# Kernel tuning notes

Measured on AMD Instinct MI355X. Metric: run time of the kernel, lower is better.

Reference implementation:

```python
import jax, jax.numpy as jnp
import numpy as np

Q, B, DM, H, HD, MEM = 1024, 4, 1024, 16, 64, 512
KLEN = MEM + Q
MLP = 4096
SCALE = 1.0 / np.sqrt(HD)
EPS = 1e-5


def _layer_norm(x, g, b):
    m = jnp.mean(x, axis=-1, keepdims=True)
    var = jnp.mean(jnp.square(x - m), axis=-1, keepdims=True)
    return (x - m) * jax.lax.rsqrt(var + EPS) * g + b


def _rel_shift(x):
    # x: [qlen, klen, batch, heads] -> Transformer-XL relative shift
    q, k, b, h = x.shape
    x = jnp.pad(x, ((0, 0), (1, 0), (0, 0), (0, 0)))  # [q, k+1, b, h]
    x = x.reshape(k + 1, q, b, h)[1:]                  # drop first row
    return x.reshape(q, k, b, h)


def setup_inputs() -> dict:
    key = jax.random.key(0)
    ks = jax.random.split(key, 16)
    s = 0.02
    inputs = jax.random.normal(ks[0], (Q, B, DM), jnp.float32)
    r = jax.random.normal(ks[1], (KLEN, DM), jnp.float32)
    u = jax.random.normal(ks[2], (H, HD), jnp.float32) * s
    v = jax.random.normal(ks[3], (H, HD), jnp.float32) * s
    mem = jax.random.normal(ks[4], (MEM, B, DM), jnp.float32)
    # causal mask with memory: query i may attend to keys j <= i + MEM
    i = jnp.arange(Q)[:, None]
    j = jnp.arange(KLEN)[None, :]
    attn_mask = j > (i + MEM)  # True = masked
    W_qkv = jax.random.normal(ks[5], (DM, 3 * H * HD), jnp.float32) * s
    W_r = jax.random.normal(ks[6], (DM, H * HD), jnp.float32) * s
    W_o = jax.random.normal(ks[7], (H * HD, DM), jnp.float32) * s
    ln1_g = jnp.ones((DM,), jnp.float32)
    ln1_b = jnp.zeros((DM,), jnp.float32)
    ln2_g = jnp.ones((DM,), jnp.float32)
    ln2_b = jnp.zeros((DM,), jnp.float32)
    W1 = jax.random.normal(ks[8], (DM, MLP), jnp.float32) * s
    b1 = jnp.zeros((MLP,), jnp.float32)
    W2 = jax.random.normal(ks[9], (MLP, DM), jnp.float32) * s
    b2 = jnp.zeros((DM,), jnp.float32)
    return {"inputs": inputs, "r": r, "u": u, "v": v, "mem": mem,
            "attn_mask": attn_mask, "W_qkv": W_qkv, "W_r": W_r, "W_o": W_o,
            "ln1_g": ln1_g, "ln1_b": ln1_b, "ln2_g": ln2_g, "ln2_b": ln2_b,
            "W1": W1, "b1": b1, "W2": W2, "b2": b2}


def reference(inputs, r, u, v, mem, attn_mask, W_qkv, W_r, W_o,
              ln1_g, ln1_b, ln2_g, ln2_b, W1, b1, W2, b2):
    qlen = inputs.shape[0]
    cat = jnp.concatenate([mem, inputs], axis=0)      # [klen, B, DM]
    klen = cat.shape[0]
    qkv = cat @ W_qkv                                  # [klen, B, 3*H*HD]
    q_h, k_h, v_h = jnp.split(qkv, 3, axis=-1)
    q_h = q_h[-qlen:].reshape(qlen, -1, H, HD)         # [q, B, H, HD]
    k_h = k_h.reshape(klen, -1, H, HD)                 # [k, B, H, HD]
    v_h = v_h.reshape(klen, -1, H, HD)
    r_h = (r @ W_r).reshape(klen, H, HD)               # [k, H, HD]
    # content score (AC) + position score (BD, rel-shifted)
    AC = jnp.einsum('ibhd,jbhd->ijbh', q_h + u, k_h)
    BD = _rel_shift(jnp.einsum('ibhd,jhd->ijbh', q_h + v, r_h))
    score = (AC + BD) * SCALE                          # [q, k, B, H]
    score = jnp.where(attn_mask[:, :, None, None], jnp.float32(-1e30), score)
    attn = jax.nn.softmax(score, axis=1)
    ctx = jnp.einsum('ijbh,jbhd->ibhd', attn, v_h).reshape(qlen, -1, H * HD)
    y = ctx @ W_o                                      # [q, B, DM]
    x = _layer_norm(inputs + y, ln1_g, ln1_b)
    h = jax.nn.relu(x @ W1 + b1)
    y2 = h @ W2 + b2
    return _layer_norm(x + y2, ln2_g, ln2_b)
```

## Files before the change

### kernel.cpp

```cpp
#include <hip/hip_runtime.h>
#include <hip/hip_bf16.h>

typedef __hip_bfloat16 bf16;
typedef _Float16 f16;
typedef __attribute__((ext_vector_type(8))) short short8;
typedef __attribute__((ext_vector_type(4))) float f32x4;
typedef __attribute__((ext_vector_type(8))) _Float16 f16x8;
typedef __attribute__((ext_vector_type(4))) _Float16 f16x4;

#define Q_LEN 1024
#define B_SZ 4
#define DM 1024
#define H_CNT 16
#define HD 64
#define MEM_LEN 512
#define KLEN 1536
#define MLP 4096

__device__ __forceinline__ void store_c(float* p, float v) { *p = v; }
__device__ __forceinline__ void store_c(bf16* p, float v) { *p = __float2bfloat16(v); }
__device__ __forceinline__ void store_c(f16* p, float v) { *p = (f16)v; }

__device__ __forceinline__ float b2f(short s) {
  union { unsigned u; float f; } x;
  x.u = ((unsigned)(unsigned short)s) << 16;
  return x.f;
}
__device__ __forceinline__ short f2b(float f) {
  union { float f; unsigned u; } x;
  x.f = f;
  unsigned r = x.u + 0x7fff + ((x.u >> 16) & 1);
  return (short)(r >> 16);
}

__device__ __forceinline__ void gload16(const void* g, void* l) {
  __builtin_amdgcn_global_load_lds(
      (__attribute__((address_space(1))) unsigned int*)(g),
      (__attribute__((address_space(3))) unsigned int*)(l), 16, 0, 0);
}

__global__ __launch_bounds__(256) void convh_kernel(
    const float* __restrict__ X, f16* __restrict__ Y, int n4) {
  const int i = blockIdx.x * 256 + threadIdx.x;
  if (i < n4) {
    f32x4 v = *(const f32x4*)&X[(size_t)i * 4];
    f16x4 h;
#pragma unroll
    for (int j = 0; j < 4; ++j) h[j] = (f16)v[j];
    *(f16x4*)&Y[(size_t)i * 4] = h;
  }
}

__global__ __launch_bounds__(256) void convT_kernel(
    const float* __restrict__ W, f16* __restrict__ WT, int K, int N) {
  __shared__ float tile[64][65];
  const int tid = threadIdx.x;
  const int k0 = blockIdx.y * 64, n0 = blockIdx.x * 64;
  const int tn = tid & 63, tk4 = tid >> 6;
#pragma unroll
  for (int p = 0; p < 16; ++p) {
    const int kk = tk4 + p * 4;
    tile[kk][tn] = W[(size_t)(k0 + kk) * N + n0 + tn];
  }
  __syncthreads();
#pragma unroll
  for (int p = 0; p < 16; ++p) {
    const int nn = tk4 + p * 4;
    WT[(size_t)(n0 + nn) * K + k0 + tn] = (f16)tile[tn][nn];
  }
}

template <typename TC>
__global__ __launch_bounds__(256, 3) void hgemm_kernel(
    const f16* __restrict__ A, const f16* __restrict__ BT, TC* C,
    int N, int K, const float* __restrict__ bias, int relu,
    const f16* __restrict__ Aalt, TC* Calt, int split,
    TC* Cb, TC* Cbalt, int ksplit) {
  __shared__ __align__(16) f16 sA[3][128 * 32];
  __shared__ __align__(16) f16 sB[3][128 * 32];
  const int tid = threadIdx.x;
  const int w = tid >> 6, lane = tid & 63;
  const int quad = lane >> 4, m16 = lane & 15;
  const int wr = w >> 1, wc = w & 1;
  const int gx = gridDim.x;
  const int nwg = gx * gridDim.y;
  const int lin = blockIdx.y * gx + blockIdx.x;
  const int cpx = nwg >> 3;
  const int swz = (lin & 7) * cpx + (lin >> 3);
  const int bx = swz % gx;
  int by = swz / gx;
  int koff = 0, Kloc = K;
  if (ksplit == 2) {
    const int mh = gridDim.y >> 1;
    if (by >= mh) { by -= mh; koff = K >> 1; C = Cb; Calt = Cbalt; }
    Kloc = K >> 1;
  }
  const int col0 = bx * 128;
  int r0 = by * 128;
  const f16* Ause = A;
  TC* Cuse = C;
  if (r0 >= split) { Ause = Aalt; Cuse = Calt; r0 -= split; }

  const int strow = tid >> 2;
  const int schunk = tid & 3;
  const int sw = schunk ^ ((strow >> 1) & 3);
  const f16* gA0 = Ause + (size_t)(r0 + strow) * K + koff + sw * 8;
  const f16* gB0 = BT + (size_t)(col0 + strow) * K + koff + sw * 8;
  f16* ldsA0 = &sA[0][0] + (size_t)w * 512;
  f16* ldsB0 = &sB[0][0] + (size_t)w * 512;

  const int qs = quad ^ ((m16 >> 1) & 3);
  int aoff[4], boff[4];
#pragma unroll
  for (int i = 0; i < 4; ++i) {
    aoff[i] = (wr * 64 + i * 16 + m16) * 32 + qs * 8;
    boff[i] = (wc * 64 + i * 16 + m16) * 32 + qs * 8;
  }

  const int nkt = Kloc >> 5;
  f32x4 acc[4][4] = {};

  auto stage = [&](int buf, int t) {
    const int k0 = t << 5;
    const size_t bufo = (size_t)buf * 4096;
    gload16(gA0 + k0, ldsA0 + bufo);
    gload16(gA0 + (size_t)64 * K + k0, ldsA0 + bufo + 2048);
    gload16(gB0 + k0, ldsB0 + bufo);
    gload16(gB0 + (size_t)64 * K + k0, ldsB0 + bufo + 2048);
  };

  stage(0, 0);
  stage(1, 1);
  int cur = 0;
  for (int t = 0; t < nkt; ++t) {
    if (t + 1 < nkt) {
      asm volatile("s_waitcnt vmcnt(4)" ::: "memory");
    } else {
      asm volatile("s_waitcnt vmcnt(0)" ::: "memory");
    }
    __builtin_amdgcn_s_barrier();
    if (t + 2 < nkt) {
      int nb = cur + 2;
      if (nb >= 3) nb -= 3;
      stage(nb, t + 2);
    }
    f16x8 af[4], bfr[4];
#pragma unroll
    for (int i = 0; i < 4; ++i) af[i] = *(const f16x8*)&sA[cur][aoff[i]];
#pragma unroll
    for (int i = 0; i < 4; ++i) bfr[i] = *(const f16x8*)&sB[cur][boff[i]];
    __builtin_amdgcn_s_setprio(1);
#pragma unroll
    for (int mi = 0; mi < 4; ++mi)
#pragma unroll
      for (int ni = 0; ni < 4; ++ni)
        acc[mi][ni] = __builtin_amdgcn_mfma_f32_16x16x32_f16(
            af[mi], bfr[ni], acc[mi][ni], 0, 0, 0);
    __builtin_amdgcn_s_setprio(0);
    cur = (cur + 1 == 3) ? 0 : cur + 1;
  }

#pragma unroll
  for (int mi = 0; mi < 4; ++mi) {
    const int row = r0 + wr * 64 + mi * 16 + quad * 4;
#pragma unroll
    for (int ni = 0; ni < 4; ++ni) {
      const int col = col0 + wc * 64 + ni * 16 + m16;
      const float bv = bias ? bias[col] : 0.f;
#pragma unroll
      for (int rg = 0; rg < 4; ++rg) {
        float vv = acc[mi][ni][rg] + bv;
        if (relu) vv = vv > 0.f ? vv : 0.f;
        store_c(&Cuse[(size_t)(row + rg) * N + col], vv);
      }
    }
  }
}

__global__ __launch_bounds__(256, 4) void fattn_kernel(
    const bf16* __restrict__ qkvp,
    const bf16* __restrict__ rhp,
    const float* __restrict__ u, const float* __restrict__ v,
    f16* __restrict__ ctxh) {
  const int lin = blockIdx.x;
  const int p = lin & 63;
  const int b = p & 3, h = p >> 2;
  const int i0 = (15 - (lin >> 6)) * 64;
  const int tid = threadIdx.x;
  const int w = tid >> 6, lane = tid & 63;
  const int quad = lane >> 4, m16 = lane & 15;

  __shared__ short sVt[64 * 40];
  __shared__ short sR[96 * 72];
  __shared__ short sProb[64 * 40];

  const short* qkv = (const short*)qkvp;
  const short* rh  = (const short*)rhp;

  short8 aQu0, aQu1, aQv0, aQv1;
  {
    const size_t qro = ((size_t)(512 + i0 + w * 16 + m16) * 4 + b) * 3072 + h * 64 + quad * 8;
    short8 qa = *(const short8*)&qkv[qro];
    short8 qb = *(const short8*)&qkv[qro + 32];
    const float* up = u + h * 64 + quad * 8;
    const float* vp = v + h * 64 + quad * 8;
#pragma unroll
    for (int j = 0; j < 8; ++j) {
      const float qaf = b2f(qa[j]), qbf = b2f(qb[j]);
      aQu0[j] = f2b(qaf + up[j]);
      aQu1[j] = f2b(qbf + up[j + 32]);
      aQv0[j] = f2b(qaf + vp[j]);
      aQv1[j] = f2b(qbf + vp[j + 32]);
    }
  }

  const int st_row = tid >> 3, st_d0 = (tid & 7) * 8;
  const int vj = lane & 31, vd0 = w * 16 + (lane >> 5) * 8;

#pragma unroll
  for (int p_ = 0; p_ < 3; ++p_) {
    int t = 960 - i0 + p_ * 32 + st_row;
    t = t > 1535 ? 1535 : t;
    *(short8*)&sR[(p_ * 32 + st_row) * 72 + st_d0] =
        *(const short8*)&rh[(size_t)t * 1024 + h * 64 + st_d0];
  }
  {
    short8 v8 = *(const short8*)&qkv[((size_t)vj * 4 + b) * 3072 + 2048 + h * 64 + vd0];
#pragma unroll
    for (int q = 0; q < 8; ++q) sVt[(vd0 + q) * 40 + vj] = v8[q];
  }
  short8 rKf[4];
#pragma unroll
  for (int n0i = 0; n0i < 2; ++n0i) {
    const size_t kro = ((size_t)(n0i * 16 + m16) * 4 + b) * 3072 + 1024 + h * 64 + quad * 8;
    rKf[n0i * 2] = *(const short8*)&qkv[kro];
    rKf[n0i * 2 + 1] = *(const short8*)&qkv[kro + 32];
  }

  short8 ones;
#pragma unroll
  for (int q = 0; q < 8; ++q) ones[q] = (short)0x3F80;

  f32x4 O[4] = {};
  f32x4 L = {};
  float m = -1e30f;
  int bk = 0;
  int tnext = 1056 - i0;

  const int n_kt = ((i0 + 575) >> 5) + 1;
  for (int kt = 0; kt < n_kt; ++kt) {
    const int j0 = kt * 32;
    const bool pf = (kt + 1 < n_kt);
    __syncthreads();

    short8 nV, nR;
    if (pf) {
      nV = *(const short8*)&qkv[((size_t)(j0 + 32 + vj) * 4 + b) * 3072 + 2048 + h * 64 + vd0];
      int t = tnext + st_row;
      t = t > 1535 ? 1535 : t;
      nR = *(const short8*)&rh[(size_t)t * 1024 + h * 64 + st_d0];
    }

    f32x4 ac[2];
#pragma unroll
    for (int n0i = 0; n0i < 2; ++n0i) {
      f32x4 a = {};
      a = __builtin_amdgcn_mfma_f32_16x16x32_bf16(aQu0, rKf[n0i * 2], a, 0, 0, 0);
      a = __builtin_amdgcn_mfma_f32_16x16x32_bf16(aQu1, rKf[n0i * 2 + 1], a, 0, 0, 0);
      ac[n0i] = a;
    }
    if (pf) {
#pragma unroll
      for (int n0i = 0; n0i < 2; ++n0i) {
        const size_t kro = ((size_t)(j0 + 32 + n0i * 16 + m16) * 4 + b) * 3072 + 1024 + h * 64 + quad * 8;
        rKf[n0i * 2] = *(const short8*)&qkv[kro];
        rKf[n0i * 2 + 1] = *(const short8*)&qkv[kro + 32];
      }
    }

    f32x4 pb[3];
#pragma unroll
    for (int pt = 0; pt < 3; ++pt) {
      const int p0 = 48 - 16 * w + 16 * pt;
      int pr = bk + p0;
      if (pr >= 96) pr -= 96;
      int row = pr + m16;
      if (row >= 96) row -= 96;
      const short8 bR0 = *(const short8*)&sR[row * 72 + quad * 8];
      const short8 bR1 = *(const short8*)&sR[row * 72 + 32 + quad * 8];
      f32x4 pf_ = {};
      pf_ = __builtin_amdgcn_mfma_f32_16x16x32_bf16(aQv0, bR0, pf_, 0, 0, 0);
      pf_ = __builtin_amdgcn_mfma_f32_16x16x32_bf16(aQv1, bR1, pf_, 0, 0, 0);
      pb[pt] = pf_;
    }

    float S0[4], S1[4];
    float mxl = -1e30f;
#pragma unroll
    for (int rg = 0; rg < 4; ++rg) {
      const int rloc = quad * 4 + rg;
      const int irow = i0 + w * 16 + rloc;
      const int c0 = m16 - rloc + 15;
      const int src = (lane & 48) | (c0 & 15);
      const float t0 = __shfl(pb[0][rg], src);
      const float t1 = __shfl(pb[1][rg], src);
      const float t2 = __shfl(pb[2][rg], src);
      const float p0v = (c0 < 16) ? t0 : t1;
      const float p1v = (c0 < 16) ? t1 : t2;
      float s0 = (ac[0][rg] + p0v) * 0.125f;
      float s1 = (ac[1][rg] + p1v) * 0.125f;
      if (j0 + m16 > irow + 512) s0 = -1e30f;
      if (j0 + 16 + m16 > irow + 512) s1 = -1e30f;
      S0[rg] = s0;
      S1[rg] = s1;
      mxl = fmaxf(mxl, fmaxf(s0, s1));
    }
    mxl = fmaxf(mxl, __shfl_xor(mxl, 1));
    mxl = fmaxf(mxl, __shfl_xor(mxl, 2));
    mxl = fmaxf(mxl, __shfl_xor(mxl, 4));
    mxl = fmaxf(mxl, __shfl_xor(mxl, 8));
    mxl = fmaxf(mxl, __shfl_xor(mxl, 16));
    mxl = fmaxf(mxl, __shfl_xor(mxl, 32));
    const float mnew = fmaxf(m, mxl);
    const float al = __expf(m - mnew);
    m = mnew;
#pragma unroll
    for (int rg = 0; rg < 4; ++rg) {
      const int rloc = quad * 4 + rg;
      sProb[(w * 16 + rloc) * 40 + m16] = f2b(__expf(S0[rg] - mnew));
      sProb[(w * 16 + rloc) * 40 + 16 + m16] = f2b(__expf(S1[rg] - mnew));
    }
#pragma unroll
    for (int d0i = 0; d0i < 4; ++d0i)
#pragma unroll
      for (int rg = 0; rg < 4; ++rg) O[d0i][rg] *= al;
#pragma unroll
    for (int rg = 0; rg < 4; ++rg) L[rg] *= al;

    const short8 aP = *(const short8*)&sProb[(w * 16 + m16) * 40 + quad * 8];
    L = __builtin_amdgcn_mfma_f32_16x16x32_bf16(aP, ones, L, 0, 0, 0);
#pragma unroll
    for (int d0i = 0; d0i < 4; ++d0i) {
      const short8 bV = *(const short8*)&sVt[(d0i * 16 + m16) * 40 + quad * 8];
      O[d0i] = __builtin_amdgcn_mfma_f32_16x16x32_bf16(aP, bV, O[d0i], 0, 0, 0);
    }

    __syncthreads();
    if (pf) {
#pragma unroll
      for (int q = 0; q < 8; ++q) sVt[(vd0 + q) * 40 + vj] = nV[q];
      *(short8*)&sR[(bk + st_row) * 72 + st_d0] = nR;
    }
    bk += 32;
    if (bk >= 96) bk = 0;
    tnext += 32;
  }

#pragma unroll
  for (int d0i = 0; d0i < 4; ++d0i) {
#pragma unroll
    for (int rg = 0; rg < 4; ++rg) {
      const int irow = i0 + w * 16 + quad * 4 + rg;
      ctxh[((size_t)irow * 4 + b) * 1024 + h * 64 + d0i * 16 + m16] =
          (f16)(O[d0i][rg] / L[rg]);
    }
  }
}

__global__ __launch_bounds__(256) void ln1_kernel(
    const f16* __restrict__ ya, const f16* __restrict__ yb,
    const float* __restrict__ inp, const float* __restrict__ g,
    const float* __restrict__ beta, f16* __restrict__ xh) {
  const int r = blockIdx.x, tid = threadIdx.x;
  __shared__ float red[256];
  float t[4];
  float s = 0.f;
#pragma unroll
  for (int q = 0; q < 4; ++q) {
    int c = tid + q * 256;
    t[q] = (float)ya[(size_t)r * DM + c] + (float)yb[(size_t)r * DM + c] +
           inp[(size_t)r * DM + c];
    s += t[q];
  }
  red[tid] = s;
  __syncthreads();
  for (int st = 128; st > 0; st >>= 1) {
    if (tid < st) red[tid] += red[tid + st];
    __syncthreads();
  }
  const float mean = red[0] * (1.f / DM);
  __syncthreads();
  float vs = 0.f;
#pragma unroll
  for (int q = 0; q < 4; ++q) {
    float d0 = t[q] - mean;
    vs += d0 * d0;
  }
  red[tid] = vs;
  __syncthreads();
  for (int st = 128; st > 0; st >>= 1) {
    if (tid < st) red[tid] += red[tid + st];
    __syncthreads();
  }
  const float rstd = rsqrtf(red[0] * (1.f / DM) + 1e-5f);
#pragma unroll
  for (int q = 0; q < 4; ++q) {
    int c = tid + q * 256;
    const float val = (t[q] - mean) * rstd * g[c] + beta[c];
    xh[(size_t)r * DM + c] = (f16)val;
  }
}

__global__ __launch_bounds__(256) void ln2_kernel(
    const f16* __restrict__ xh, const f16* __restrict__ y2a,
    const f16* __restrict__ y2b, const float* __restrict__ b2,
    const float* __restrict__ g, const float* __restrict__ beta,
    float* __restrict__ out) {
  const int r = blockIdx.x, tid = threadIdx.x;
  __shared__ float red[256];
  float t[4];
  float s = 0.f;
#pragma unroll
  for (int q = 0; q < 4; ++q) {
    int c = tid + q * 256;
    t[q] = (float)xh[(size_t)r * DM + c] + (float)y2a[(size_t)r * DM + c] +
           (float)y2b[(size_t)r * DM + c] + b2[c];
    s += t[q];
  }
  red[tid] = s;
  __syncthreads();
  for (int st = 128; st > 0; st >>= 1) {
    if (tid < st) red[tid] += red[tid + st];
    __syncthreads();
  }
  const float mean = red[0] * (1.f / DM);
  __syncthreads();
  float vs = 0.f;
#pragma unroll
  for (int q = 0; q < 4; ++q) {
    float d0 = t[q] - mean;
    vs += d0 * d0;
  }
  red[tid] = vs;
  __syncthreads();
  for (int st = 128; st > 0; st >>= 1) {
    if (tid < st) red[tid] += red[tid + st];
    __syncthreads();
  }
  const float rstd = rsqrtf(red[0] * (1.f / DM) + 1e-5f);
#pragma unroll
  for (int q = 0; q < 4; ++q) {
    int c = tid + q * 256;
    out[(size_t)r * DM + c] = (t[q] - mean) * rstd * g[c] + beta[c];
  }
}

extern "C" void kernel_launch(void* const* d_in, const int* in_sizes, int n_in,
                              void* d_out, int out_size, void* d_ws, size_t ws_size,
                              hipStream_t stream) {
  const int o = (n_in >= 17) ? 1 : 0;
  const float* inputs = (const float*)d_in[0];
  const float* r      = (const float*)d_in[1];
  const float* u      = (const float*)d_in[2];
  const float* v      = (const float*)d_in[3];
  const float* memp   = (const float*)d_in[4];
  const float* W_qkv  = (const float*)d_in[5 + o];
  const float* W_r    = (const float*)d_in[6 + o];
  const float* W_o    = (const float*)d_in[7 + o];
  const float* ln1_g  = (const float*)d_in[8 + o];
  const float* ln1_b  = (const float*)d_in[9 + o];
  const float* ln2_g  = (const float*)d_in[10 + o];
  const float* ln2_b  = (const float*)d_in[11 + o];
  const float* W1     = (const float*)d_in[12 + o];
  const float* b1     = (const float*)d_in[13 + o];
  const float* W2     = (const float*)d_in[14 + o];
  const float* b2     = (const float*)d_in[15 + o];

  char* ws = (char*)d_ws;
  f16*  WqkvT = (f16*)(ws);
  f16*  r16   = (f16*)(ws + 6291456);
  f16*  WrT   = (f16*)(ws + 9437184);
  bf16* qkv   = (bf16*)(ws + 11534336);
  bf16* rh    = (bf16*)(ws + 49283072);
  f16*  cat_h = (f16*)d_out;
  f16*  ctx_h = (f16*)(ws);
  f16*  WoT   = (f16*)(ws + 8388608);
  f16*  ya    = (f16*)(ws + 10485760);
  f16*  yb    = (f16*)(ws + 18874368);
  f16*  x_h   = (f16*)(ws + 27262976);
  f16*  W1T   = (f16*)(ws + 35651584);
  f16*  h_hi  = (f16*)(ws);
  f16*  h_lo  = (f16*)d_out;
  f16*  W2T   = (f16*)(ws + 44040192);
  f16*  y2a   = (f16*)(ws + 18874368);
  f16*  y2b   = (f16*)(ws + 35651584);

  dim3 blk(256);
  const int BIG = 1 << 30;

  convh_kernel<<<dim3(2048), blk, 0, stream>>>(memp, cat_h, 524288);
  convh_kernel<<<dim3(4096), blk, 0, stream>>>(inputs, cat_h + (size_t)2048 * 1024, 1048576);
  convh_kernel<<<dim3(1536), blk, 0, stream>>>(r, r16, 393216);
  convT_kernel<<<dim3(48, 16), blk, 0, stream>>>(W_qkv, WqkvT, 1024, 3072);
  convT_kernel<<<dim3(16, 16), blk, 0, stream>>>(W_r, WrT, 1024, 1024);
  hgemm_kernel<bf16><<<dim3(24, 48), blk, 0, stream>>>(
      cat_h, WqkvT, qkv, 3072, 1024, nullptr, 0,
      nullptr, nullptr, BIG, nullptr, nullptr, 1);
  hgemm_kernel<bf16><<<dim3(8, 12), blk, 0, stream>>>(
      r16, WrT, rh, 1024, 1024, nullptr, 0,
      nullptr, nullptr, BIG, nullptr, nullptr, 1);
  fattn_kernel<<<dim3(1024), blk, 0, stream>>>(qkv, rh, u, v, ctx_h);

  convT_kernel<<<dim3(16, 16), blk, 0, stream>>>(W_o, WoT, 1024, 1024);
  hgemm_kernel<f16><<<dim3(8, 64), blk, 0, stream>>>(
      ctx_h, WoT, ya, 1024, 1024, nullptr, 0,
      nullptr, nullptr, BIG, yb, nullptr, 2);
  ln1_kernel<<<dim3(4096), blk, 0, stream>>>(ya, yb, inputs, ln1_g, ln1_b, x_h);
  convT_kernel<<<dim3(64, 16), blk, 0, stream>>>(W1, W1T, 1024, 4096);
  hgemm_kernel<f16><<<dim3(32, 32), blk, 0, stream>>>(
      x_h, W1T, h_lo, 4096, 1024, b1, 1,
      x_h + (size_t)2048 * 1024, h_hi, 2048, nullptr, nullptr, 1);
  convT_kernel<<<dim3(16, 64), blk, 0, stream>>>(W2, W2T, 4096, 1024);
  hgemm_kernel<f16><<<dim3(8, 64), blk, 0, stream>>>(
      h_lo, W2T, y2a, 1024, 4096, nullptr, 0,
      h_hi, y2a + (size_t)2048 * 1024, 2048,
      y2b, y2b + (size_t)2048 * 1024, 2);
  ln2_kernel<<<dim3(4096), blk, 0, stream>>>(x_h, y2a, y2b, b2, ln2_g, ln2_b,
                                             (float*)d_out);
}
```

Before: 483.4 us.

## Double-buffer attention tiles, lazy softmax rescale, two-stage GEMM pipeline with higher occupancy

The attention kernel double-buffers the V tile and enlarges the R ring to 128 rows so one of the two per-iteration barriers can be dropped. It evaluates the causal mask only on tiles that may cross the diagonal, and rescales the running max only when it grows by more than a threshold. The GEMM switches from a three-stage to a two-stage LDS pipeline to cut shared memory and target four blocks per CU. The GEMM loses prefetch depth, and the lazy rescale lets unnormalised probabilities grow larger before accumulation.

```diff
diff --git a/kernel.cpp b/kernel.cpp
--- a/kernel.cpp
+++ b/kernel.cpp
@@ -71,13 +71,13 @@
 }
 
 template <typename TC>
-__global__ __launch_bounds__(256, 3) void hgemm_kernel(
+__global__ __launch_bounds__(256, 4) void hgemm_kernel(
     const f16* __restrict__ A, const f16* __restrict__ BT, TC* C,
     int N, int K, const float* __restrict__ bias, int relu,
     const f16* __restrict__ Aalt, TC* Calt, int split,
     TC* Cb, TC* Cbalt, int ksplit) {
-  __shared__ __align__(16) f16 sA[3][128 * 32];
-  __shared__ __align__(16) f16 sB[3][128 * 32];
+  __shared__ __align__(16) f16 sA[2][128 * 32];
+  __shared__ __align__(16) f16 sB[2][128 * 32];
   const int tid = threadIdx.x;
   const int w = tid >> 6, lane = tid & 63;
   const int quad = lane >> 4, m16 = lane & 15;
@@ -130,20 +130,11 @@
   };
 
   stage(0, 0);
-  stage(1, 1);
   int cur = 0;
   for (int t = 0; t < nkt; ++t) {
-    if (t + 1 < nkt) {
-      asm volatile("s_waitcnt vmcnt(4)" ::: "memory");
-    } else {
-      asm volatile("s_waitcnt vmcnt(0)" ::: "memory");
-    }
+    asm volatile("s_waitcnt vmcnt(0)" ::: "memory");
     __builtin_amdgcn_s_barrier();
-    if (t + 2 < nkt) {
-      int nb = cur + 2;
-      if (nb >= 3) nb -= 3;
-      stage(nb, t + 2);
-    }
+    if (t + 1 < nkt) stage(cur ^ 1, t + 1);
     f16x8 af[4], bfr[4];
 #pragma unroll
     for (int i = 0; i < 4; ++i) af[i] = *(const f16x8*)&sA[cur][aoff[i]];
@@ -157,7 +148,7 @@
         acc[mi][ni] = __builtin_amdgcn_mfma_f32_16x16x32_f16(
             af[mi], bfr[ni], acc[mi][ni], 0, 0, 0);
     __builtin_amdgcn_s_setprio(0);
-    cur = (cur + 1 == 3) ? 0 : cur + 1;
+    cur ^= 1;
   }
 
 #pragma unroll
@@ -190,8 +181,8 @@
   const int w = tid >> 6, lane = tid & 63;
   const int quad = lane >> 4, m16 = lane & 15;
 
-  __shared__ short sVt[64 * 40];
-  __shared__ short sR[96 * 72];
+  __shared__ short sVt[2][64 * 40];
+  __shared__ short sR[128 * 72];
   __shared__ short sProb[64 * 40];
 
   const short* qkv = (const short*)qkvp;
@@ -227,7 +218,7 @@
   {
     short8 v8 = *(const short8*)&qkv[((size_t)vj * 4 + b) * 3072 + 2048 + h * 64 + vd0];
 #pragma unroll
-    for (int q = 0; q < 8; ++q) sVt[(vd0 + q) * 40 + vj] = v8[q];
+    for (int q = 0; q < 8; ++q) sVt[0][(vd0 + q) * 40 + vj] = v8[q];
   }
   short8 rKf[4];
 #pragma unroll
@@ -251,6 +242,7 @@
   for (int kt = 0; kt < n_kt; ++kt) {
     const int j0 = kt * 32;
     const bool pf = (kt + 1 < n_kt);
+    const int vbuf = kt & 1;
     __syncthreads();
 
     short8 nV, nR;
@@ -282,10 +274,7 @@
 #pragma unroll
     for (int pt = 0; pt < 3; ++pt) {
       const int p0 = 48 - 16 * w + 16 * pt;
-      int pr = bk + p0;
-      if (pr >= 96) pr -= 96;
-      int row = pr + m16;
-      if (row >= 96) row -= 96;
+      const int row = (bk + p0 + m16) & 127;
       const short8 bR0 = *(const short8*)&sR[row * 72 + quad * 8];
       const short8 bR1 = *(const short8*)&sR[row * 72 + 32 + quad * 8];
       f32x4 pf_ = {};
@@ -294,12 +283,12 @@
       pb[pt] = pf_;
     }
 
+    const bool needmask = (j0 + 31 > i0 + w * 16 + 512);
     float S0[4], S1[4];
     float mxl = -1e30f;
 #pragma unroll
     for (int rg = 0; rg < 4; ++rg) {
       const int rloc = quad * 4 + rg;
-      const int irow = i0 + w * 16 + rloc;
       const int c0 = m16 - rloc + 15;
       const int src = (lane & 48) | (c0 & 15);
       const float t0 = __shfl(pb[0][rg], src);
@@ -309,8 +298,11 @@
       const float p1v = (c0 < 16) ? t1 : t2;
       float s0 = (ac[0][rg] + p0v) * 0.125f;
       float s1 = (ac[1][rg] + p1v) * 0.125f;
-      if (j0 + m16 > irow + 512) s0 = -1e30f;
-      if (j0 + 16 + m16 > irow + 512) s1 = -1e30f;
+      if (needmask) {
+        const int irow = i0 + w * 16 + rloc;
+        if (j0 + m16 > irow + 512) s0 = -1e30f;
+        if (j0 + 16 + m16 > irow + 512) s1 = -1e30f;
+      }
       S0[rg] = s0;
       S1[rg] = s1;
       mxl = fmaxf(mxl, fmaxf(s0, s1));
@@ -321,38 +313,37 @@
     mxl = fmaxf(mxl, __shfl_xor(mxl, 8));
     mxl = fmaxf(mxl, __shfl_xor(mxl, 16));
     mxl = fmaxf(mxl, __shfl_xor(mxl, 32));
-    const float mnew = fmaxf(m, mxl);
-    const float al = __expf(m - mnew);
-    m = mnew;
+    if (mxl > m + 8.f) {
+      const float al = __expf(m - mxl);
+      m = mxl;
+#pragma unroll
+      for (int d0i = 0; d0i < 4; ++d0i)
+#pragma unroll
+        for (int rg = 0; rg < 4; ++rg) O[d0i][rg] *= al;
+#pragma unroll
+      for (int rg = 0; rg < 4; ++rg) L[rg] *= al;
+    }
 #pragma unroll
     for (int rg = 0; rg < 4; ++rg) {
       const int rloc = quad * 4 + rg;
-      sProb[(w * 16 + rloc) * 40 + m16] = f2b(__expf(S0[rg] - mnew));
-      sProb[(w * 16 + rloc) * 40 + 16 + m16] = f2b(__expf(S1[rg] - mnew));
-    }
-#pragma unroll
-    for (int d0i = 0; d0i < 4; ++d0i)
-#pragma unroll
-      for (int rg = 0; rg < 4; ++rg) O[d0i][rg] *= al;
-#pragma unroll
-    for (int rg = 0; rg < 4; ++rg) L[rg] *= al;
+      sProb[(w * 16 + rloc) * 40 + m16] = f2b(__expf(S0[rg] - m));
+      sProb[(w * 16 + rloc) * 40 + 16 + m16] = f2b(__expf(S1[rg] - m));
+    }
 
     const short8 aP = *(const short8*)&sProb[(w * 16 + m16) * 40 + quad * 8];
     L = __builtin_amdgcn_mfma_f32_16x16x32_bf16(aP, ones, L, 0, 0, 0);
 #pragma unroll
     for (int d0i = 0; d0i < 4; ++d0i) {
-      const short8 bV = *(const short8*)&sVt[(d0i * 16 + m16) * 40 + quad * 8];
+      const short8 bV = *(const short8*)&sVt[vbuf][(d0i * 16 + m16) * 40 + quad * 8];
       O[d0i] = __builtin_amdgcn_mfma_f32_16x16x32_bf16(aP, bV, O[d0i], 0, 0, 0);
     }
 
-    __syncthreads();
     if (pf) {
 #pragma unroll
-      for (int q = 0; q < 8; ++q) sVt[(vd0 + q) * 40 + vj] = nV[q];
-      *(short8*)&sR[(bk + st_row) * 72 + st_d0] = nR;
-    }
-    bk += 32;
-    if (bk >= 96) bk = 0;
+      for (int q = 0; q < 8; ++q) sVt[vbuf ^ 1][(vd0 + q) * 40 + vj] = nV[q];
+      *(short8*)&sR[(((bk + 96) & 127) + st_row) * 72 + st_d0] = nR;
+    }
+    bk = (bk + 32) & 127;
     tnext += 32;
   }
 
```

After: 478.3 us. Within noise of the previous version (-1.0%).

## Merge conversion launches and switch GEMM to double-buffered LDS pipeline

Applied to the files above, without the earlier changes.

The three fp32-to-fp16 conversion launches are merged into one kernel, and the five weight transpose-convert launches are grouped into two multi-matrix kernels. The W1 and W2 transposes now run right after attention instead of being interleaved with the later GEMMs. The GEMM drops from a three-stage LDS ring with partial vmcnt waits to a two-stage buffer with a full wait every K-step, and raises the occupancy hint from 3 to 4 waves per SIMD. This trades load/compute overlap for lower LDS use and more resident workgroups, and cuts kernel launch count.

```diff
diff --git a/kernel.cpp b/kernel.cpp
--- a/kernel.cpp
+++ b/kernel.cpp
@@ -39,23 +39,37 @@
       (__attribute__((address_space(3))) unsigned int*)(l), 16, 0, 0);
 }
 
-__global__ __launch_bounds__(256) void convh_kernel(
-    const float* __restrict__ X, f16* __restrict__ Y, int n4) {
-  const int i = blockIdx.x * 256 + threadIdx.x;
-  if (i < n4) {
-    f32x4 v = *(const f32x4*)&X[(size_t)i * 4];
-    f16x4 h;
-#pragma unroll
-    for (int j = 0; j < 4; ++j) h[j] = (f16)v[j];
-    *(f16x4*)&Y[(size_t)i * 4] = h;
-  }
-}
-
-__global__ __launch_bounds__(256) void convT_kernel(
-    const float* __restrict__ W, f16* __restrict__ WT, int K, int N) {
+__global__ __launch_bounds__(256) void convh3_kernel(
+    const float* __restrict__ X0, const float* __restrict__ X1,
+    const float* __restrict__ X2, f16* __restrict__ Y0,
+    f16* __restrict__ Y1, f16* __restrict__ Y2) {
+  const int blk = blockIdx.x, tid = threadIdx.x;
+  const float* X;
+  f16* Y;
+  int i;
+  if (blk < 2048) { X = X0; Y = Y0; i = blk * 256 + tid; }
+  else if (blk < 6144) { X = X1; Y = Y1; i = (blk - 2048) * 256 + tid; }
+  else { X = X2; Y = Y2; i = (blk - 6144) * 256 + tid; }
+  f32x4 v = *(const f32x4*)&X[(size_t)i * 4];
+  f16x4 h;
+#pragma unroll
+  for (int j = 0; j < 4; ++j) h[j] = (f16)v[j];
+  *(f16x4*)&Y[(size_t)i * 4] = h;
+}
+
+__global__ __launch_bounds__(256) void convTm_kernel(
+    const float* W0, f16* T0, int K0, int N0, int nx0,
+    int s1, const float* W1p, f16* T1, int K1, int N1, int nx1,
+    int s2, const float* W2p, f16* T2, int K2, int N2, int nx2) {
   __shared__ float tile[64][65];
-  const int tid = threadIdx.x;
-  const int k0 = blockIdx.y * 64, n0 = blockIdx.x * 64;
+  const int blk = blockIdx.x, tid = threadIdx.x;
+  const float* W;
+  f16* WT;
+  int K, N, nx, local;
+  if (blk < s1) { W = W0; WT = T0; K = K0; N = N0; nx = nx0; local = blk; }
+  else if (blk < s2) { W = W1p; WT = T1; K = K1; N = N1; nx = nx1; local = blk - s1; }
+  else { W = W2p; WT = T2; K = K2; N = N2; nx = nx2; local = blk - s2; }
+  const int n0 = (local % nx) * 64, k0 = (local / nx) * 64;
   const int tn = tid & 63, tk4 = tid >> 6;
 #pragma unroll
   for (int p = 0; p < 16; ++p) {
@@ -71,13 +85,13 @@
 }
 
 template <typename TC>
-__global__ __launch_bounds__(256, 3) void hgemm_kernel(
+__global__ __launch_bounds__(256, 4) void hgemm_kernel(
     const f16* __restrict__ A, const f16* __restrict__ BT, TC* C,
     int N, int K, const float* __restrict__ bias, int relu,
     const f16* __restrict__ Aalt, TC* Calt, int split,
     TC* Cb, TC* Cbalt, int ksplit) {
-  __shared__ __align__(16) f16 sA[3][128 * 32];
-  __shared__ __align__(16) f16 sB[3][128 * 32];
+  __shared__ __align__(16) f16 sA[2][128 * 32];
+  __shared__ __align__(16) f16 sB[2][128 * 32];
   const int tid = threadIdx.x;
   const int w = tid >> 6, lane = tid & 63;
   const int quad = lane >> 4, m16 = lane & 15;
@@ -130,20 +144,11 @@
   };
 
   stage(0, 0);
-  stage(1, 1);
   int cur = 0;
   for (int t = 0; t < nkt; ++t) {
-    if (t + 1 < nkt) {
-      asm volatile("s_waitcnt vmcnt(4)" ::: "memory");
-    } else {
-      asm volatile("s_waitcnt vmcnt(0)" ::: "memory");
-    }
+    asm volatile("s_waitcnt vmcnt(0)" ::: "memory");
     __builtin_amdgcn_s_barrier();
-    if (t + 2 < nkt) {
-      int nb = cur + 2;
-      if (nb >= 3) nb -= 3;
-      stage(nb, t + 2);
-    }
+    if (t + 1 < nkt) stage(cur ^ 1, t + 1);
     f16x8 af[4], bfr[4];
 #pragma unroll
     for (int i = 0; i < 4; ++i) af[i] = *(const f16x8*)&sA[cur][aoff[i]];
@@ -157,7 +162,7 @@
         acc[mi][ni] = __builtin_amdgcn_mfma_f32_16x16x32_f16(
             af[mi], bfr[ni], acc[mi][ni], 0, 0, 0);
     __builtin_amdgcn_s_setprio(0);
-    cur = (cur + 1 == 3) ? 0 : cur + 1;
+    cur ^= 1;
   }
 
 #pragma unroll
@@ -498,11 +503,12 @@
   dim3 blk(256);
   const int BIG = 1 << 30;
 
-  convh_kernel<<<dim3(2048), blk, 0, stream>>>(memp, cat_h, 524288);
-  convh_kernel<<<dim3(4096), blk, 0, stream>>>(inputs, cat_h + (size_t)2048 * 1024, 1048576);
-  convh_kernel<<<dim3(1536), blk, 0, stream>>>(r, r16, 393216);
-  convT_kernel<<<dim3(48, 16), blk, 0, stream>>>(W_qkv, WqkvT, 1024, 3072);
-  convT_kernel<<<dim3(16, 16), blk, 0, stream>>>(W_r, WrT, 1024, 1024);
+  convh3_kernel<<<dim3(7680), blk, 0, stream>>>(
+      memp, inputs, r, cat_h, cat_h + (size_t)2048 * 1024, r16);
+  convTm_kernel<<<dim3(1024), blk, 0, stream>>>(
+      W_qkv, WqkvT, 1024, 3072, 48,
+      768, W_r, WrT, 1024, 1024, 16,
+      1024, nullptr, nullptr, 0, 0, 1);
   hgemm_kernel<bf16><<<dim3(24, 48), blk, 0, stream>>>(
       cat_h, WqkvT, qkv, 3072, 1024, nullptr, 0,
       nullptr, nullptr, BIG, nullptr, nullptr, 1);
@@ -511,16 +517,17 @@
       nullptr, nullptr, BIG, nullptr, nullptr, 1);
   fattn_kernel<<<dim3(1024), blk, 0, stream>>>(qkv, rh, u, v, ctx_h);
 
-  convT_kernel<<<dim3(16, 16), blk, 0, stream>>>(W_o, WoT, 1024, 1024);
+  convTm_kernel<<<dim3(2304), blk, 0, stream>>>(
+      W_o, WoT, 1024, 1024, 16,
+      256, W1, W1T, 1024, 4096, 64,
+      1280, W2, W2T, 4096, 1024, 16);
   hgemm_kernel<f16><<<dim3(8, 64), blk, 0, stream>>>(
       ctx_h, WoT, ya, 1024, 1024, nullptr, 0,
       nullptr, nullptr, BIG, yb, nullptr, 2);
   ln1_kernel<<<dim3(4096), blk, 0, stream>>>(ya, yb, inputs, ln1_g, ln1_b, x_h);
-  convT_kernel<<<dim3(64, 16), blk, 0, stream>>>(W1, W1T, 1024, 4096);
   hgemm_kernel<f16><<<dim3(32, 32), blk, 0, stream>>>(
       x_h, W1T, h_lo, 4096, 1024, b1, 1,
       x_h + (size_t)2048 * 1024, h_hi, 2048, nullptr, nullptr, 1);
-  convT_kernel<<<dim3(16, 64), blk, 0, stream>>>(W2, W2T, 4096, 1024);
   hgemm_kernel<f16><<<dim3(8, 64), blk, 0, stream>>>(
       h_lo, W2T, y2a, 1024, 4096, nullptr, 0,
       h_hi, y2a + (size_t)2048 * 1024, 2048,
```

New measurement: 459.4 us. -5.0%, faster.
